# Kernel tuning notes

Hardware: AMD Instinct MI355X
Metric: run time of the kernel (lower is better)

## Reference

```python
import jax, jax.numpy as jnp
import numpy as np

N_NODES = 50000
N_EDGES = 600000
D = 128
LAYERS = 2


def setup_inputs() -> dict:
    key = jax.random.key(0)
    ks = jax.random.split(key, 7)
    row = jax.random.randint(ks[0], (N_EDGES,), 0, N_NODES, dtype=jnp.int32)
    col = jax.random.randint(ks[1], (N_EDGES,), 0, N_NODES, dtype=jnp.int32)
    vals = jax.random.normal(ks[2], (N_EDGES,), dtype=jnp.float32)
    X = jax.random.normal(ks[3], (N_NODES, D), dtype=jnp.float32)
    temps = jax.random.normal(ks[4], (LAYERS, D), dtype=jnp.float32) * 0.1
    W = jax.random.normal(ks[5], (LAYERS, D, D), dtype=jnp.float32) * (1.0 / np.sqrt(D))
    b = jax.random.normal(ks[6], (LAYERS, D), dtype=jnp.float32) * 0.01
    return {"row": row, "col": col, "vals": vals, "X": X, "temps": temps, "W": W, "b": b}


def reference(row, col, vals, X, temps, W, b):
    # Iterated: X <- relu(Linear_i(X - temp_i * (Lap @ X)))
    for i in range(LAYERS):
        # spmm via COO edge list: LX[r] = sum_e vals[e] * X[col[e]] for edges with row[e]==r
        msgs = vals[:, None] * X[col]            # [E, D] gather + scale
        LX = jax.ops.segment_sum(msgs, row, num_segments=N_NODES)  # [N, D] scatter-add
        X = X - temps[i] * LX                    # elementwise scale-subtract
        X = jax.nn.relu(X @ W[i].T + b[i])       # Linear (torch: x W^T + b) + ReLU
    return X
```

## Files before the change

kernel.cpp:

```cpp
#include <hip/hip_runtime.h>

#define N_NODES 50000
#define N_EDGES 600000
#define D 128
#define LAYERS 2
#define NAL 50048
#define CAP 48
#define NB1 256
#define EPB 2344
#define NBINS 256
#define BIN_ROWS 196
#define FRAG_CAP 32
#define PBLOCKS 6250

typedef short bf16x8 __attribute__((ext_vector_type(8)));
typedef float f32x4 __attribute__((ext_vector_type(4)));
typedef float f32x2 __attribute__((ext_vector_type(2)));

__device__ __forceinline__ ushort f2b(float f) {
  uint u = __float_as_uint(f);
  return (ushort)((u + 0x7fffu + ((u >> 16) & 1u)) >> 16);
}
__device__ __forceinline__ float b2f_lo(uint p) { return __uint_as_float(p << 16); }
__device__ __forceinline__ float b2f_hi(uint p) { return __uint_as_float(p & 0xffff0000u); }

__global__ __launch_bounds__(256) void k_bin_prep(
    const int* __restrict__ row, const int* __restrict__ col,
    const float* __restrict__ vals,
    uint2* __restrict__ staging, int* __restrict__ bcnt,
    const float* __restrict__ X, const float* __restrict__ W,
    ushort* __restrict__ Xb, ushort* __restrict__ Wb, uint* __restrict__ Xf8) {
  const int blk = blockIdx.x;
  const int t = threadIdx.x;
  if (blk < NB1) {
    __shared__ int lcur[NBINS];
    lcur[t] = 0;
    __syncthreads();
    const int e0 = blk * EPB;
    for (int i = t; i < EPB; i += 256) {
      int e = e0 + i;
      if (e < N_EDGES) {
        int r = row[e];
        int bin = r / BIN_ROWS;
        int slot = atomicAdd(&lcur[bin], 1);
        if (slot < FRAG_CAP) {
          uint cv = ((uint)f2b(vals[e]) << 16) | (uint)col[e];
          staging[((size_t)blk * NBINS + bin) * FRAG_CAP + slot] =
              make_uint2(cv, (uint)r);
        }
      }
    }
    __syncthreads();
    bcnt[blk * NBINS + t] = min(lcur[t], FRAG_CAP);
  } else {
    int i = (blk - NB1) * 256 + t;
    if (i < N_NODES * D / 4) {
      float4 v = ((const float4*)X)[i];
      ushort4 o;
      o.x = f2b(v.x); o.y = f2b(v.y); o.z = f2b(v.z); o.w = f2b(v.w);
      ((ushort4*)Xb)[i] = o;
      int pk = __builtin_amdgcn_cvt_pk_fp8_f32(v.x, v.y, 0, false);
      pk = __builtin_amdgcn_cvt_pk_fp8_f32(v.z, v.w, pk, true);
      Xf8[i] = (uint)pk;
    }
    if (i < LAYERS * D * D / 4) {
      float4 v = ((const float4*)W)[i];
      ushort4 o;
      o.x = f2b(v.x); o.y = f2b(v.y); o.z = f2b(v.z); o.w = f2b(v.w);
      ((ushort4*)Wb)[i] = o;
    }
  }
}

__global__ __launch_bounds__(256) void k_scatter(
    const uint2* __restrict__ staging, const int* __restrict__ bcnt,
    int* __restrict__ counts, uint* __restrict__ ell) {
  const int b = blockIdx.x;
  const int t = threadIdx.x;
  __shared__ int lcur[BIN_ROWS];
  for (int i = t; i < BIN_ROWS; i += 256) lcur[i] = 0;
  __syncthreads();
  const int rbase = b * BIN_ROWS;
  const int n = bcnt[t * NBINS + b];
  const uint2* frag = staging + ((size_t)t * NBINS + b) * FRAG_CAP;
  for (int k = 0; k < n; ++k) {
    uint2 E = frag[k];
    int rl = (int)E.y - rbase;
    int slot = atomicAdd(&lcur[rl], 1);
    if (slot < CAP) ell[(size_t)E.y * CAP + slot] = E.x;
  }
  __syncthreads();
  for (int i = t; i < BIN_ROWS; i += 256) {
    int r = rbase + i;
    if (r < NAL) counts[r] = lcur[i];
  }
}

__global__ __launch_bounds__(256) void k_layer(
    const int* __restrict__ counts, const uint* __restrict__ ell,
    const ushort* __restrict__ Xin, const uchar* __restrict__ Xg8,
    const ushort* __restrict__ Wb, const float* __restrict__ bias,
    const float* __restrict__ temps_l,
    ushort* __restrict__ Yb, uchar* __restrict__ Yf8,
    float* __restrict__ Yf, int store_f32) {
  __shared__ ushort Xs[16][136];
  const int t = threadIdx.x;

  {
    const int nloc = t >> 4;
    const int c = t & 15;
    const int g = blockIdx.x * 16 + nloc;
    const uint* ep = ell + (size_t)g * CAP;
    int cnt = counts[g];
    if (cnt > CAP) cnt = CAP;
    float a0 = 0.f, a1 = 0.f, a2 = 0.f, a3 = 0.f;
    float a4 = 0.f, a5 = 0.f, a6 = 0.f, a7 = 0.f;
#define EDGE_FMA(v, q)                                                  \
    {                                                                   \
      f32x2 f0 = __builtin_amdgcn_cvt_pk_f32_fp8((q).x, false);         \
      f32x2 f1 = __builtin_amdgcn_cvt_pk_f32_fp8((q).x, true);          \
      f32x2 f2 = __builtin_amdgcn_cvt_pk_f32_fp8((q).y, false);         \
      f32x2 f3 = __builtin_amdgcn_cvt_pk_f32_fp8((q).y, true);          \
      a0 = fmaf(v, f0.x, a0); a1 = fmaf(v, f0.y, a1);                   \
      a2 = fmaf(v, f1.x, a2); a3 = fmaf(v, f1.y, a3);                   \
      a4 = fmaf(v, f2.x, a4); a5 = fmaf(v, f2.y, a5);                   \
      a6 = fmaf(v, f3.x, a6); a7 = fmaf(v, f3.y, a7);                   \
    }
    uint4 ea = *(const uint4*)(ep);
    uint4 eb = *(const uint4*)(ep + 4);
    int j = 0;
    for (; j + 8 <= cnt; j += 8) {
      uint4 na = *(const uint4*)(ep + j + 8);
      uint4 nb = *(const uint4*)(ep + j + 12);
      uint2 q0 = *(const uint2*)(Xg8 + ((size_t)(ea.x & 0xFFFFu) << 7) + c * 8);
      uint2 q1 = *(const uint2*)(Xg8 + ((size_t)(ea.y & 0xFFFFu) << 7) + c * 8);
      uint2 q2 = *(const uint2*)(Xg8 + ((size_t)(ea.z & 0xFFFFu) << 7) + c * 8);
      uint2 q3 = *(const uint2*)(Xg8 + ((size_t)(ea.w & 0xFFFFu) << 7) + c * 8);
      uint2 q4 = *(const uint2*)(Xg8 + ((size_t)(eb.x & 0xFFFFu) << 7) + c * 8);
      uint2 q5 = *(const uint2*)(Xg8 + ((size_t)(eb.y & 0xFFFFu) << 7) + c * 8);
      uint2 q6 = *(const uint2*)(Xg8 + ((size_t)(eb.z & 0xFFFFu) << 7) + c * 8);
      uint2 q7 = *(const uint2*)(Xg8 + ((size_t)(eb.w & 0xFFFFu) << 7) + c * 8);
      EDGE_FMA(b2f_hi(ea.x), q0); EDGE_FMA(b2f_hi(ea.y), q1);
      EDGE_FMA(b2f_hi(ea.z), q2); EDGE_FMA(b2f_hi(ea.w), q3);
      EDGE_FMA(b2f_hi(eb.x), q4); EDGE_FMA(b2f_hi(eb.y), q5);
      EDGE_FMA(b2f_hi(eb.z), q6); EDGE_FMA(b2f_hi(eb.w), q7);
      ea = na; eb = nb;
    }
    if (j + 4 <= cnt) {
      uint2 q0 = *(const uint2*)(Xg8 + ((size_t)(ea.x & 0xFFFFu) << 7) + c * 8);
      uint2 q1 = *(const uint2*)(Xg8 + ((size_t)(ea.y & 0xFFFFu) << 7) + c * 8);
      uint2 q2 = *(const uint2*)(Xg8 + ((size_t)(ea.z & 0xFFFFu) << 7) + c * 8);
      uint2 q3 = *(const uint2*)(Xg8 + ((size_t)(ea.w & 0xFFFFu) << 7) + c * 8);
      EDGE_FMA(b2f_hi(ea.x), q0); EDGE_FMA(b2f_hi(ea.y), q1);
      EDGE_FMA(b2f_hi(ea.z), q2); EDGE_FMA(b2f_hi(ea.w), q3);
      ea = eb;
      j += 4;
    }
    for (; j < cnt; ++j) {
      uint e = ep[j];
      uint2 q = *(const uint2*)(Xg8 + ((size_t)(e & 0xFFFFu) << 7) + c * 8);
      EDGE_FMA(b2f_hi(e), q);
    }
#undef EDGE_FMA
    uint4 pr = *(const uint4*)(Xin + ((size_t)g << 7) + c * 8);
    float4 t0 = *(const float4*)(temps_l + c * 8);
    float4 t1 = *(const float4*)(temps_l + c * 8 + 4);
    uint r0 = (uint)f2b(b2f_lo(pr.x) - t0.x * a0) | ((uint)f2b(b2f_hi(pr.x) - t0.y * a1) << 16);
    uint r1 = (uint)f2b(b2f_lo(pr.y) - t0.z * a2) | ((uint)f2b(b2f_hi(pr.y) - t0.w * a3) << 16);
    uint r2 = (uint)f2b(b2f_lo(pr.z) - t1.x * a4) | ((uint)f2b(b2f_hi(pr.z) - t1.y * a5) << 16);
    uint r3 = (uint)f2b(b2f_lo(pr.w) - t1.z * a6) | ((uint)f2b(b2f_hi(pr.w) - t1.w * a7) << 16);
    *(uint4*)&Xs[nloc][c * 8] = make_uint4(r0, r1, r2, r3);
  }
  __syncthreads();

  const int wave = t >> 6;
  const int lane = t & 63;
  const int lr = lane & 15;
  const int kg = lane >> 4;

  bf16x8 a0 = *(const bf16x8*)&Xs[lr][0 + kg * 8];
  bf16x8 a1 = *(const bf16x8*)&Xs[lr][32 + kg * 8];
  bf16x8 a2 = *(const bf16x8*)&Xs[lr][64 + kg * 8];
  bf16x8 a3 = *(const bf16x8*)&Xs[lr][96 + kg * 8];

  const int crow = kg * 4;
  #pragma unroll
  for (int q = 0; q < 2; ++q) {
    const int nt = wave * 2 + q;
    const ushort* wp = Wb + ((size_t)(nt * 16 + lr) << 7) + kg * 8;
    bf16x8 b0 = *(const bf16x8*)(wp);
    bf16x8 b1 = *(const bf16x8*)(wp + 32);
    bf16x8 b2 = *(const bf16x8*)(wp + 64);
    bf16x8 b3 = *(const bf16x8*)(wp + 96);
    f32x4 acc = {0.f, 0.f, 0.f, 0.f};
    acc = __builtin_amdgcn_mfma_f32_16x16x32_bf16(a0, b0, acc, 0, 0, 0);
    acc = __builtin_amdgcn_mfma_f32_16x16x32_bf16(a1, b1, acc, 0, 0, 0);
    acc = __builtin_amdgcn_mfma_f32_16x16x32_bf16(a2, b2, acc, 0, 0, 0);
    acc = __builtin_amdgcn_mfma_f32_16x16x32_bf16(a3, b3, acc, 0, 0, 0);
    const int col = nt * 16 + lr;
    const float bv = bias[col];
    if (store_f32) {
      #pragma unroll
      for (int r = 0; r < 4; ++r) {
        int grow = blockIdx.x * 16 + crow + r;
        if (grow < N_NODES)
          Yf[((size_t)grow << 7) + col] = fmaxf(acc[r] + bv, 0.f);
      }
    } else {
      #pragma unroll
      for (int r = 0; r < 4; ++r) {
        int grow = blockIdx.x * 16 + crow + r;
        float o = fmaxf(acc[r] + bv, 0.f);
        Yb[((size_t)grow << 7) + col] = f2b(o);
        int pk = __builtin_amdgcn_cvt_pk_fp8_f32(o, o, 0, false);
        Yf8[((size_t)grow << 7) + col] = (uchar)(pk & 0xff);
      }
    }
  }
}

extern "C" void kernel_launch(void* const* d_in, const int* in_sizes, int n_in,
                              void* d_out, int out_size, void* d_ws, size_t ws_size,
                              hipStream_t stream) {
  const int*   row   = (const int*)d_in[0];
  const int*   col   = (const int*)d_in[1];
  const float* vals  = (const float*)d_in[2];
  const float* X     = (const float*)d_in[3];
  const float* temps = (const float*)d_in[4];
  const float* W     = (const float*)d_in[5];
  const float* b     = (const float*)d_in[6];
  float* Y = (float*)d_out;

  int*    counts  = (int*)d_ws;
  int*    bcnt    = counts + NAL;
  uint2*  staging = (uint2*)(bcnt + NB1 * NBINS);
  uint*   ell     = (uint*)(staging + (size_t)NB1 * NBINS * FRAG_CAP);
  ushort* Xb      = (ushort*)(ell + (size_t)NAL * CAP);
  ushort* Yb      = Xb + (size_t)NAL * D;
  ushort* Wb      = Yb + (size_t)NAL * D;
  uchar*  Xf8     = (uchar*)(Wb + LAYERS * D * D);
  uchar*  Yf8     = Xf8 + (size_t)NAL * D;

  const int lblocks = NAL / 16;

  k_bin_prep<<<NB1 + PBLOCKS, 256, 0, stream>>>(row, col, vals, staging, bcnt,
                                                X, W, Xb, Wb, (uint*)Xf8);
  k_scatter<<<NBINS, 256, 0, stream>>>(staging, bcnt, counts, ell);

  k_layer<<<lblocks, 256, 0, stream>>>(counts, ell, Xb, Xf8, Wb, b, temps,
                                       Yb, Yf8, nullptr, 0);
  k_layer<<<lblocks, 256, 0, stream>>>(counts, ell, Yb, Yf8, Wb + D * D, b + D,
                                       temps + D, nullptr, nullptr, Y, 1);
}
```

Baseline: 87.55 us.

## Sort nodes by degree so each layer block processes similar-degree rows

Adds a per-bin degree histogram in the scatter kernel, a single-block prefix-sum kernel, and a permutation kernel that orders node indices by in-degree. The layer kernels then pick their 16 rows through this permutation, so rows in a wave have similar edge counts and less lane divergence or imbalance. In exchange it adds two extra launches, including a serial single-block prefix kernel. Output writes also become scattered by row, and spatial locality of rows within a block is lost.

Result: slower. 96.23 us (+9.9%).

```diff
diff --git a/kernel.cpp b/kernel.cpp
--- a/kernel.cpp
+++ b/kernel.cpp
@@ -74,11 +74,13 @@
 
 __global__ __launch_bounds__(256) void k_scatter(
     const uint2* __restrict__ staging, const int* __restrict__ bcnt,
-    int* __restrict__ counts, uint* __restrict__ ell) {
+    int* __restrict__ counts, uint* __restrict__ ell, int* __restrict__ hist) {
   const int b = blockIdx.x;
   const int t = threadIdx.x;
   __shared__ int lcur[BIN_ROWS];
+  __shared__ int h[64];
   for (int i = t; i < BIN_ROWS; i += 256) lcur[i] = 0;
+  if (t < 64) h[t] = 0;
   __syncthreads();
   const int rbase = b * BIN_ROWS;
   const int n = bcnt[t * NBINS + b];
@@ -92,24 +94,79 @@
   __syncthreads();
   for (int i = t; i < BIN_ROWS; i += 256) {
     int r = rbase + i;
-    if (r < NAL) counts[r] = lcur[i];
+    if (r < NAL) {
+      int c = lcur[i];
+      counts[r] = c;
+      atomicAdd(&h[min(c, CAP)], 1);
+    }
+  }
+  __syncthreads();
+  if (t < 64) hist[b * 64 + t] = h[t];
+}
+
+__global__ __launch_bounds__(256) void k_prefix(const int* __restrict__ hist,
+                                                int* __restrict__ pre) {
+  __shared__ int sh[NBINS * 64];
+  __shared__ int degstart[64];
+  const int t = threadIdx.x;
+  for (int i = t; i < NBINS * 64; i += 256) sh[i] = hist[i];
+  __syncthreads();
+  if (t < 64) {
+    int s = 0;
+    for (int b = 0; b < NBINS; ++b) s += sh[b * 64 + t];
+    degstart[t] = s;
+  }
+  __syncthreads();
+  if (t == 0) {
+    int run = 0;
+    for (int d = 0; d < 64; ++d) { int v = degstart[d]; degstart[d] = run; run += v; }
+  }
+  __syncthreads();
+  if (t < 64) {
+    int run = degstart[t];
+    for (int b = 0; b < NBINS; ++b) {
+      pre[b * 64 + t] = run;
+      run += sh[b * 64 + t];
+    }
+  }
+}
+
+__global__ __launch_bounds__(256) void k_perm(const int* __restrict__ counts,
+                                              const int* __restrict__ pre,
+                                              int* __restrict__ perm) {
+  const int b = blockIdx.x;
+  const int t = threadIdx.x;
+  __shared__ int lcur[64];
+  if (t < 64) lcur[t] = pre[b * 64 + t];
+  __syncthreads();
+  const int rbase = b * BIN_ROWS;
+  for (int i = t; i < BIN_ROWS; i += 256) {
+    int r = rbase + i;
+    if (r < NAL) {
+      int d = min(counts[r], CAP);
+      int pos = atomicAdd(&lcur[d], 1);
+      perm[pos] = r;
+    }
   }
 }
 
 __global__ __launch_bounds__(256) void k_layer(
     const int* __restrict__ counts, const uint* __restrict__ ell,
+    const int* __restrict__ perm,
     const ushort* __restrict__ Xin, const uchar* __restrict__ Xg8,
     const ushort* __restrict__ Wb, const float* __restrict__ bias,
     const float* __restrict__ temps_l,
     ushort* __restrict__ Yb, uchar* __restrict__ Yf8,
     float* __restrict__ Yf, int store_f32) {
   __shared__ ushort Xs[16][136];
-  const int t = threadIdx.x;
+  __shared__ int ps[16];
+  const int t = threadIdx.x;
+  if (t < 16) ps[t] = perm[blockIdx.x * 16 + t];
 
   {
     const int nloc = t >> 4;
     const int c = t & 15;
-    const int g = blockIdx.x * 16 + nloc;
+    const int g = perm[blockIdx.x * 16 + nloc];
     const uint* ep = ell + (size_t)g * CAP;
     int cnt = counts[g];
     if (cnt > CAP) cnt = CAP;
@@ -202,14 +259,14 @@
     if (store_f32) {
       #pragma unroll
       for (int r = 0; r < 4; ++r) {
-        int grow = blockIdx.x * 16 + crow + r;
+        int grow = ps[crow + r];
         if (grow < N_NODES)
           Yf[((size_t)grow << 7) + col] = fmaxf(acc[r] + bv, 0.f);
       }
     } else {
       #pragma unroll
       for (int r = 0; r < 4; ++r) {
-        int grow = blockIdx.x * 16 + crow + r;
+        int grow = ps[crow + r];
         float o = fmaxf(acc[r] + bv, 0.f);
         Yb[((size_t)grow << 7) + col] = f2b(o);
         int pk = __builtin_amdgcn_cvt_pk_fp8_f32(o, o, 0, false);
@@ -232,8 +289,11 @@
   float* Y = (float*)d_out;
 
   int*    counts  = (int*)d_ws;
-  int*    bcnt    = counts + NAL;
-  uint2*  staging = (uint2*)(bcnt + NB1 * NBINS);
+  int*    perm    = counts + NAL;
+  int*    bcnt    = perm + NAL;
+  int*    hist    = bcnt + NB1 * NBINS;
+  int*    pre     = hist + NBINS * 64;
+  uint2*  staging = (uint2*)(pre + NBINS * 64);
   uint*   ell     = (uint*)(staging + (size_t)NB1 * NBINS * FRAG_CAP);
   ushort* Xb      = (ushort*)(ell + (size_t)NAL * CAP);
   ushort* Yb      = Xb + (size_t)NAL * D;
@@ -245,10 +305,12 @@
 
   k_bin_prep<<<NB1 + PBLOCKS, 256, 0, stream>>>(row, col, vals, staging, bcnt,
                                                 X, W, Xb, Wb, (uint*)Xf8);
-  k_scatter<<<NBINS, 256, 0, stream>>>(staging, bcnt, counts, ell);
-
-  k_layer<<<lblocks, 256, 0, stream>>>(counts, ell, Xb, Xf8, Wb, b, temps,
+  k_scatter<<<NBINS, 256, 0, stream>>>(staging, bcnt, counts, ell, hist);
+  k_prefix<<<1, 256, 0, stream>>>(hist, pre);
+  k_perm<<<NBINS, 256, 0, stream>>>(counts, pre, perm);
+
+  k_layer<<<lblocks, 256, 0, stream>>>(counts, ell, perm, Xb, Xf8, Wb, b, temps,
                                        Yb, Yf8, nullptr, 0);
-  k_layer<<<lblocks, 256, 0, stream>>>(counts, ell, Yb, Yf8, Wb + D * D, b + D,
-                                       temps + D, nullptr, nullptr, Y, 1);
-}
+  k_layer<<<lblocks, 256, 0, stream>>>(counts, ell, perm, Yb, Yf8, Wb + D * D,
+                                       b + D, temps + D, nullptr, nullptr, Y, 1);
+}
```
